# Performance work log

Hardware: AMD Instinct MI355X
Metric: run time of the kernel (lower is better)

The kernel has to match this reference:

```python
import jax, jax.numpy as jnp
import numpy as np

B, S, D = 2, 2048, 4096
H, HKV, HD = 32, 8, 128          # heads, kv heads, head_dim
G = H // HKV                      # query groups per kv head
THETA = 10000.0


def setup_inputs() -> dict:
    key = jax.random.key(0)
    ks = jax.random.split(key, 6)
    s = 0.02
    return {
        "hidden_states": jax.random.normal(ks[0], (B, S, D), jnp.float32),
        "position_ids": jnp.broadcast_to(jnp.arange(S, dtype=jnp.int32), (B, S)),
        "attention_mask": jnp.ones((B, S), jnp.int32),
        "Wq": jax.random.normal(ks[1], (D, H * HD), jnp.float32) * s,
        "Wk": jax.random.normal(ks[2], (D, HKV * HD), jnp.float32) * s,
        "Wv": jax.random.normal(ks[3], (D, HKV * HD), jnp.float32) * s,
        "Wo": jax.random.normal(ks[4], (H * HD, D), jnp.float32) * s,
    }


def _rope_neox(x, positions):
    # x: [B, S, h, HD]; neox style: rotate halves
    half = HD // 2
    inv_freq = 1.0 / (THETA ** (jnp.arange(0, half, dtype=jnp.float32) / half))
    freqs = positions.astype(jnp.float32)[..., None] * inv_freq  # [B,S,half]
    cos = jnp.cos(freqs)[:, :, None, :]
    sin = jnp.sin(freqs)[:, :, None, :]
    x1, x2 = x[..., :half], x[..., half:]
    return jnp.concatenate([x1 * cos - x2 * sin, x2 * cos + x1 * sin], axis=-1)


def reference(hidden_states, position_ids, attention_mask, Wq, Wk, Wv, Wo):
    q = (hidden_states @ Wq).reshape(B, S, H, HD)
    k = (hidden_states @ Wk).reshape(B, S, HKV, HD)
    v = (hidden_states @ Wv).reshape(B, S, HKV, HD)

    q = _rope_neox(q, position_ids)
    k = _rope_neox(k, position_ids)

    # GQA: group query heads onto kv heads
    qg = q.reshape(B, S, HKV, G, HD)
    scale = HD ** -0.5
    scores = jnp.einsum("bqhgd,bkhd->bhgqk", qg, k) * scale  # [B,HKV,G,S,S]

    causal = jnp.tril(jnp.ones((S, S), bool))
    mask = causal[None, None, None] & (attention_mask[:, None, None, None, :] > 0)
    scores = jnp.where(mask, scores, jnp.finfo(scores.dtype).min)
    probs = jax.nn.softmax(scores, axis=-1)

    ctx = jnp.einsum("bhgqk,bkhd->bqhgd", probs, v).reshape(B, S, H * HD)
    return ctx @ Wo
```

## Files before the change

### kernel.cpp

```cpp
#include <hip/hip_runtime.h>
#include <hip/hip_bf16.h>
#include <cstdint>
#include <cstddef>

#define BB 2
#define SS 2048
#define DD 4096
#define HH 32
#define HKV 8
#define HDIM 128
#define NQKV 6144

typedef __attribute__((ext_vector_type(8))) short bf16x8;
typedef __attribute__((ext_vector_type(4))) float f32x4;

#define GLOAD_LDS16(g, l) __builtin_amdgcn_global_load_lds( \
    (const __attribute__((address_space(1))) void*)(g), \
    (__attribute__((address_space(3))) void*)(l), 16, 0, 0)

__global__ void cast_bf16_kernel(const float* __restrict__ in,
                                 __hip_bfloat16* __restrict__ out, int n4) {
  int i = blockIdx.x * 256 + threadIdx.x;
  if (i >= n4) return;
  float4 v = ((const float4*)in)[i];
  union { __hip_bfloat16 h[4]; short4 s4; } u;
  u.h[0] = __float2bfloat16(v.x);
  u.h[1] = __float2bfloat16(v.y);
  u.h[2] = __float2bfloat16(v.z);
  u.h[3] = __float2bfloat16(v.w);
  ((short4*)out)[i] = u.s4;
}

__global__ void transpose_cast4_kernel(const float* __restrict__ Wq,
                                       const float* __restrict__ Wk,
                                       const float* __restrict__ Wv,
                                       const float* __restrict__ Wo,
                                       __hip_bfloat16* __restrict__ WqkvT,
                                       __hip_bfloat16* __restrict__ WoT) {
  __shared__ float tile[32][33];
  int id = blockIdx.x;
  const float* W; __hip_bfloat16* WT; int C, bx, by;
  if (id < 16384)      { W = Wq; WT = WqkvT;                         C = 4096; int l = id;         bx = l & 127; by = l >> 7; }
  else if (id < 20480) { W = Wk; WT = WqkvT + (size_t)4096 * 4096;   C = 1024; int l = id - 16384; bx = l & 31;  by = l >> 5; }
  else if (id < 24576) { W = Wv; WT = WqkvT + (size_t)5120 * 4096;   C = 1024; int l = id - 20480; bx = l & 31;  by = l >> 5; }
  else                 { W = Wo; WT = WoT;                           C = 4096; int l = id - 24576; bx = l & 127; by = l >> 7; }
  const int R = 4096;
  int c0 = bx * 32, r0 = by * 32;
  int tx = threadIdx.x, ty = threadIdx.y;
#pragma unroll
  for (int i = 0; i < 32; i += 8)
    tile[ty + i][tx] = W[(size_t)(r0 + ty + i) * C + c0 + tx];
  __syncthreads();
#pragma unroll
  for (int i = 0; i < 32; i += 8)
    WT[(size_t)(c0 + ty + i) * R + r0 + tx] = __float2bfloat16(tile[tx][ty + i]);
}

__global__ void vt_kernel(const __hip_bfloat16* __restrict__ QKV,
                          __hip_bfloat16* __restrict__ VT) {
  __shared__ __hip_bfloat16 tile[32][33];
  int c0 = blockIdx.x * 32;
  int r0 = blockIdx.y * 32;
  int tx = threadIdx.x, ty = threadIdx.y;
#pragma unroll
  for (int i = 0; i < 32; i += 8)
    tile[ty + i][tx] = QKV[(size_t)(r0 + ty + i) * NQKV + 5120 + c0 + tx];
  __syncthreads();
#pragma unroll
  for (int i = 0; i < 32; i += 8) {
    int r = r0 + tx;
    int c = c0 + ty + i;
    VT[((size_t)(r >> 11) * 1024 + c) * SS + (r & 2047)] = tile[tx][ty + i];
  }
}

__global__ void rope_kernel(__hip_bfloat16* __restrict__ QKV,
                            const int* __restrict__ pos_ids) {
  int r = blockIdx.x;
  float fpos = (float)pos_ids[r];
  __hip_bfloat16* row = QKV + (size_t)r * NQKV;
  for (int p = threadIdx.x; p < 2560; p += 256) {
    int base, i;
    if (p < 2048) { base = (p >> 6) * HDIM; i = p & 63; }
    else { int q = p - 2048; base = DD + (q >> 6) * HDIM; i = q & 63; }
    float inv = exp2f(-(float)i * 0.20762050593046015f);
    float f = fpos * inv;
    float c = cosf(f), s = sinf(f);
    float x1 = __bfloat162float(row[base + i]);
    float x2 = __bfloat162float(row[base + i + 64]);
    row[base + i]      = __float2bfloat16(x1 * c - x2 * s);
    row[base + i + 64] = __float2bfloat16(x2 * c + x1 * s);
  }
}

template <int OUTF32>
__global__ __launch_bounds__(256) void gemm_bt_kernel(const __hip_bfloat16* __restrict__ A,
                                                      const __hip_bfloat16* __restrict__ BT,
                                                      void* __restrict__ Cout,
                                                      int M, int N, int K) {
  __shared__ alignas(16) __hip_bfloat16 As[128 * 32];
  __shared__ alignas(16) __hip_bfloat16 Bs[128 * 32];
  int bn = blockIdx.x, bm = blockIdx.y;
  int tid = threadIdx.x, wave = tid >> 6, lane = tid & 63;
  int lr = lane & 15, lq = lane >> 4;
  int wm = (wave >> 1) * 64, wn = (wave & 1) * 64;
  int row0 = bm * 128, col0 = bn * 128;
  int swz = lq ^ ((lr >> 1) & 3);
  f32x4 acc[4][4] = {};
  for (int k0 = 0; k0 < K; k0 += 32) {
    __syncthreads();
#pragma unroll
    for (int i = 0; i < 2; ++i) {
      int c = tid + i * 256;
      int r = c >> 2, cl = c & 3;
      int cg = cl ^ ((r >> 1) & 3);
      GLOAD_LDS16(A + (size_t)(row0 + r) * K + k0 + cg * 8, As + (size_t)c * 8);
      GLOAD_LDS16(BT + (size_t)(col0 + r) * K + k0 + cg * 8, Bs + (size_t)c * 8);
    }
    __syncthreads();
    bf16x8 af[4], bfb[4];
#pragma unroll
    for (int mt = 0; mt < 4; ++mt)
      af[mt] = *(const bf16x8*)(As + ((wm + mt * 16 + lr) * 4 + swz) * 8);
#pragma unroll
    for (int nt = 0; nt < 4; ++nt)
      bfb[nt] = *(const bf16x8*)(Bs + ((wn + nt * 16 + lr) * 4 + swz) * 8);
#pragma unroll
    for (int mt = 0; mt < 4; ++mt)
#pragma unroll
      for (int nt = 0; nt < 4; ++nt)
        acc[mt][nt] = __builtin_amdgcn_mfma_f32_16x16x32_bf16(af[mt], bfb[nt], acc[mt][nt], 0, 0, 0);
  }
#pragma unroll
  for (int mt = 0; mt < 4; ++mt)
#pragma unroll
    for (int nt = 0; nt < 4; ++nt)
#pragma unroll
      for (int r = 0; r < 4; ++r) {
        int row = row0 + wm + mt * 16 + lq * 4 + r;
        int col = col0 + wn + nt * 16 + lr;
        if (OUTF32) ((float*)Cout)[(size_t)row * N + col] = acc[mt][nt][r];
        else ((__hip_bfloat16*)Cout)[(size_t)row * N + col] = __float2bfloat16(acc[mt][nt][r]);
      }
}

#define PSTRIDE 72
__global__ __launch_bounds__(256) void attn_kernel(const __hip_bfloat16* __restrict__ QKV,
                                                   const __hip_bfloat16* __restrict__ VT,
                                                   __hip_bfloat16* __restrict__ Ctx) {
  __shared__ alignas(16) __hip_bfloat16 Ks[64 * 128];
  __shared__ alignas(16) __hip_bfloat16 Vs[128 * 64];
  __shared__ alignas(16) __hip_bfloat16 Ps[4][32 * PSTRIDE];
  int h = blockIdx.y, b = blockIdx.z;
  int hkv = h >> 2;
  int tid = threadIdx.x, wave = tid >> 6, lane = tid & 63;
  int lr = lane & 15, lq = lane >> 4;
  const __hip_bfloat16* Kbase = QKV + (size_t)b * SS * NQKV + DD + hkv * HDIM;
  const __hip_bfloat16* Vbase = VT + (size_t)(b * HKV + hkv) * HDIM * SS;
  const float scale = 0.08838834764831845f;

  for (int half = 0; half < 2; ++half) {
    int qt = half ? (15 - blockIdx.x) : blockIdx.x;
    int q0 = qt * 128 + wave * 32;

    bf16x8 qfrag[2][4];
#pragma unroll
    for (int mt = 0; mt < 2; ++mt) {
      const __hip_bfloat16* qrow = QKV + (size_t)(b * SS + q0 + mt * 16 + lr) * NQKV + h * HDIM;
#pragma unroll
      for (int ks = 0; ks < 4; ++ks) qfrag[mt][ks] = *(const bf16x8*)(qrow + ks * 32 + lq * 8);
    }

    f32x4 accO[2][8] = {};
    float m_r[2][4], l_r[2][4];
#pragma unroll
    for (int mt = 0; mt < 2; ++mt)
#pragma unroll
      for (int r = 0; r < 4; ++r) { m_r[mt][r] = -1e30f; l_r[mt][r] = 0.f; }

    int kv_end = qt * 128 + 128;
    for (int kv0 = 0; kv0 < kv_end; kv0 += 64) {
      __syncthreads();
#pragma unroll
      for (int i = 0; i < 4; ++i) {
        int c = tid + i * 256;
        int r = c >> 4, cl = c & 15, cg = cl ^ (r & 15);
        GLOAD_LDS16(Kbase + (size_t)(kv0 + r) * NQKV + cg * 8, Ks + (size_t)c * 8);
      }
#pragma unroll
      for (int i = 0; i < 4; ++i) {
        int c = tid + i * 256;
        int r = c >> 3, cl = c & 7, cg = cl ^ (r & 7);
        GLOAD_LDS16(Vbase + (size_t)r * SS + kv0 + cg * 8, Vs + (size_t)c * 8);
      }
      __syncthreads();

      f32x4 sc[2][4] = {};
#pragma unroll
      for (int nt = 0; nt < 4; ++nt)
#pragma unroll
        for (int ks = 0; ks < 4; ++ks) {
          int cl = (ks * 4 + lq) ^ lr;
          bf16x8 kf = *(const bf16x8*)(Ks + ((nt * 16 + lr) * 16 + cl) * 8);
#pragma unroll
          for (int mt = 0; mt < 2; ++mt)
            sc[mt][nt] = __builtin_amdgcn_mfma_f32_16x16x32_bf16(qfrag[mt][ks], kf, sc[mt][nt], 0, 0, 0);
        }

      if (kv0 + 64 > qt * 128) {
#pragma unroll
        for (int mt = 0; mt < 2; ++mt)
#pragma unroll
          for (int nt = 0; nt < 4; ++nt)
#pragma unroll
            for (int r = 0; r < 4; ++r) {
              float v = sc[mt][nt][r] * scale;
              int qp = q0 + mt * 16 + lq * 4 + r;
              int kp = kv0 + nt * 16 + lr;
              sc[mt][nt][r] = (kp > qp) ? -1e30f : v;
            }
      } else {
#pragma unroll
        for (int mt = 0; mt < 2; ++mt)
#pragma unroll
          for (int nt = 0; nt < 4; ++nt)
#pragma unroll
            for (int r = 0; r < 4; ++r) sc[mt][nt][r] *= scale;
      }

      float alpha[2][4];
#pragma unroll
      for (int mt = 0; mt < 2; ++mt)
#pragma unroll
        for (int r = 0; r < 4; ++r) {
          float mx = fmaxf(fmaxf(sc[mt][0][r], sc[mt][1][r]), fmaxf(sc[mt][2][r], sc[mt][3][r]));
#pragma unroll
          for (int d = 1; d < 16; d <<= 1) mx = fmaxf(mx, __shfl_xor(mx, d));
          float mnew = fmaxf(m_r[mt][r], mx);
          alpha[mt][r] = __expf(m_r[mt][r] - mnew);
          m_r[mt][r] = mnew;
        }
#pragma unroll
      for (int mt = 0; mt < 2; ++mt)
#pragma unroll
        for (int nt = 0; nt < 4; ++nt)
#pragma unroll
          for (int r = 0; r < 4; ++r) sc[mt][nt][r] = __expf(sc[mt][nt][r] - m_r[mt][r]);
#pragma unroll
      for (int mt = 0; mt < 2; ++mt)
#pragma unroll
        for (int r = 0; r < 4; ++r) {
          float sm = (sc[mt][0][r] + sc[mt][1][r]) + (sc[mt][2][r] + sc[mt][3][r]);
#pragma unroll
          for (int d = 1; d < 16; d <<= 1) sm += __shfl_xor(sm, d);
          l_r[mt][r] = l_r[mt][r] * alpha[mt][r] + sm;
        }
#pragma unroll
      for (int mt = 0; mt < 2; ++mt)
#pragma unroll
        for (int t = 0; t < 8; ++t)
#pragma unroll
          for (int r = 0; r < 4; ++r) accO[mt][t][r] *= alpha[mt][r];

      __hip_bfloat16* P = Ps[wave];
#pragma unroll
      for (int mt = 0; mt < 2; ++mt)
#pragma unroll
        for (int nt = 0; nt < 4; ++nt)
#pragma unroll
          for (int r = 0; r < 4; ++r)
            P[(mt * 16 + lq * 4 + r) * PSTRIDE + nt * 16 + lr] = __float2bfloat16(sc[mt][nt][r]);

#pragma unroll
      for (int ks2 = 0; ks2 < 2; ++ks2) {
        bf16x8 pf[2];
#pragma unroll
        for (int mt = 0; mt < 2; ++mt)
          pf[mt] = *(const bf16x8*)(P + (mt * 16 + lr) * PSTRIDE + ks2 * 32 + lq * 8);
#pragma unroll
        for (int t = 0; t < 8; ++t) {
          int cl = (ks2 * 4 + lq) ^ (lr & 7);
          bf16x8 vf = *(const bf16x8*)(Vs + ((t * 16 + lr) * 8 + cl) * 8);
#pragma unroll
          for (int mt = 0; mt < 2; ++mt)
            accO[mt][t] = __builtin_amdgcn_mfma_f32_16x16x32_bf16(pf[mt], vf, accO[mt][t], 0, 0, 0);
        }
      }
    }

#pragma unroll
    for (int mt = 0; mt < 2; ++mt)
#pragma unroll
      for (int t = 0; t < 8; ++t)
#pragma unroll
        for (int r = 0; r < 4; ++r) {
          float o = accO[mt][t][r] / l_r[mt][r];
          int row = q0 + mt * 16 + lq * 4 + r;
          int col = h * HDIM + t * 16 + lr;
          Ctx[(size_t)(b * SS + row) * (HH * HDIM) + col] = __float2bfloat16(o);
        }
  }
}

extern "C" void kernel_launch(void* const* d_in, const int* in_sizes, int n_in,
                              void* d_out, int out_size, void* d_ws, size_t ws_size,
                              hipStream_t stream) {
  const float* X  = (const float*)d_in[0];
  const int* pos  = (const int*)d_in[1];
  const float* Wq = (const float*)d_in[3];
  const float* Wk = (const float*)d_in[4];
  const float* Wv = (const float*)d_in[5];
  const float* Wo = (const float*)d_in[6];
  float* out = (float*)d_out;

  char* ws = (char*)d_ws;
  __hip_bfloat16* Xb    = (__hip_bfloat16*)(ws);
  __hip_bfloat16* Ctx   = (__hip_bfloat16*)(ws);
  __hip_bfloat16* WqkvT = (__hip_bfloat16*)(ws + 33554432);
  __hip_bfloat16* WoT   = (__hip_bfloat16*)(ws + 83886080);
  __hip_bfloat16* QKV   = (__hip_bfloat16*)(ws + 117440512);
  __hip_bfloat16* VT    = (__hip_bfloat16*)(ws + 167772160);

  const int n4 = (BB * SS * DD) / 4;
  cast_bf16_kernel<<<dim3(n4 / 256), dim3(256), 0, stream>>>(X, Xb, n4);

  transpose_cast4_kernel<<<dim3(40960), dim3(32, 8), 0, stream>>>(Wq, Wk, Wv, Wo, WqkvT, WoT);

  gemm_bt_kernel<0><<<dim3(6144 / 128, 4096 / 128), dim3(256), 0, stream>>>(Xb, WqkvT, QKV, 4096, 6144, 4096);

  rope_kernel<<<dim3(BB * SS), dim3(256), 0, stream>>>(QKV, pos);
  vt_kernel<<<dim3(1024 / 32, 4096 / 32), dim3(32, 8), 0, stream>>>(QKV, VT);

  attn_kernel<<<dim3(SS / 256, HH, BB), dim3(256), 0, stream>>>(QKV, VT, Ctx);

  gemm_bt_kernel<1><<<dim3(4096 / 128, 4096 / 128), dim3(256), 0, stream>>>(Ctx, WoT, out, 4096, 4096, 4096);
}
```

Measured before the change: 947.8 us.

## Use 32x32x16 MFMA with BK=64 in GEMM and shrink attention query tiles

The GEMM moves from 16x16x32 MFMA tiles with a K-step of 32 to 32x32x16 MFMA tiles with a K-step of 64 and a matching XOR swizzle. This halves the barrier count per K and cuts LDS fragment reads per MFMA. The attention kernel drops from 128 to 64 query rows per block (16 per wave) and doubles the grid. It adds a swizzled P buffer and a launch bound of 4 blocks per CU, aiming for more parallelism and lower register pressure. The cost is that each K/V tile loaded into LDS is now reused by fewer query rows, so K/V traffic per query row rises.

```diff
diff --git a/kernel.cpp b/kernel.cpp
--- a/kernel.cpp
+++ b/kernel.cpp
@@ -13,6 +13,7 @@
 
 typedef __attribute__((ext_vector_type(8))) short bf16x8;
 typedef __attribute__((ext_vector_type(4))) float f32x4;
+typedef __attribute__((ext_vector_type(16))) float f32x16;
 
 #define GLOAD_LDS16(g, l) __builtin_amdgcn_global_load_lds( \
     (const __attribute__((address_space(1))) void*)(g), \
@@ -98,59 +99,64 @@
                                                       const __hip_bfloat16* __restrict__ BT,
                                                       void* __restrict__ Cout,
                                                       int M, int N, int K) {
-  __shared__ alignas(16) __hip_bfloat16 As[128 * 32];
-  __shared__ alignas(16) __hip_bfloat16 Bs[128 * 32];
+  __shared__ alignas(16) __hip_bfloat16 As[128 * 64];
+  __shared__ alignas(16) __hip_bfloat16 Bs[128 * 64];
   int bn = blockIdx.x, bm = blockIdx.y;
   int tid = threadIdx.x, wave = tid >> 6, lane = tid & 63;
-  int lr = lane & 15, lq = lane >> 4;
+  int lm = lane & 31, lh = lane >> 5;
   int wm = (wave >> 1) * 64, wn = (wave & 1) * 64;
   int row0 = bm * 128, col0 = bn * 128;
-  int swz = lq ^ ((lr >> 1) & 3);
-  f32x4 acc[4][4] = {};
-  for (int k0 = 0; k0 < K; k0 += 32) {
+  f32x16 acc[2][2] = {};
+  for (int k0 = 0; k0 < K; k0 += 64) {
     __syncthreads();
 #pragma unroll
-    for (int i = 0; i < 2; ++i) {
+    for (int i = 0; i < 4; ++i) {
       int c = tid + i * 256;
-      int r = c >> 2, cl = c & 3;
-      int cg = cl ^ ((r >> 1) & 3);
+      int r = c >> 3, cl = c & 7;
+      int cg = cl ^ (r & 7);
       GLOAD_LDS16(A + (size_t)(row0 + r) * K + k0 + cg * 8, As + (size_t)c * 8);
       GLOAD_LDS16(BT + (size_t)(col0 + r) * K + k0 + cg * 8, Bs + (size_t)c * 8);
     }
     __syncthreads();
-    bf16x8 af[4], bfb[4];
-#pragma unroll
-    for (int mt = 0; mt < 4; ++mt)
-      af[mt] = *(const bf16x8*)(As + ((wm + mt * 16 + lr) * 4 + swz) * 8);
-#pragma unroll
-    for (int nt = 0; nt < 4; ++nt)
-      bfb[nt] = *(const bf16x8*)(Bs + ((wn + nt * 16 + lr) * 4 + swz) * 8);
-#pragma unroll
-    for (int mt = 0; mt < 4; ++mt)
-#pragma unroll
-      for (int nt = 0; nt < 4; ++nt)
-        acc[mt][nt] = __builtin_amdgcn_mfma_f32_16x16x32_bf16(af[mt], bfb[nt], acc[mt][nt], 0, 0, 0);
+#pragma unroll
+    for (int ks = 0; ks < 4; ++ks) {
+      bf16x8 af[2], bfb[2];
+#pragma unroll
+      for (int mt = 0; mt < 2; ++mt) {
+        int cl = (ks * 2 + lh) ^ (lm & 7);
+        af[mt] = *(const bf16x8*)(As + (wm + mt * 32 + lm) * 64 + cl * 8);
+      }
+#pragma unroll
+      for (int nt = 0; nt < 2; ++nt) {
+        int cl = (ks * 2 + lh) ^ (lm & 7);
+        bfb[nt] = *(const bf16x8*)(Bs + (wn + nt * 32 + lm) * 64 + cl * 8);
+      }
+#pragma unroll
+      for (int mt = 0; mt < 2; ++mt)
+#pragma unroll
+        for (int nt = 0; nt < 2; ++nt)
+          acc[mt][nt] = __builtin_amdgcn_mfma_f32_32x32x16_bf16(af[mt], bfb[nt], acc[mt][nt], 0, 0, 0);
+    }
   }
 #pragma unroll
-  for (int mt = 0; mt < 4; ++mt)
-#pragma unroll
-    for (int nt = 0; nt < 4; ++nt)
-#pragma unroll
-      for (int r = 0; r < 4; ++r) {
-        int row = row0 + wm + mt * 16 + lq * 4 + r;
-        int col = col0 + wn + nt * 16 + lr;
+  for (int mt = 0; mt < 2; ++mt)
+#pragma unroll
+    for (int nt = 0; nt < 2; ++nt)
+#pragma unroll
+      for (int r = 0; r < 16; ++r) {
+        int row = row0 + wm + mt * 32 + (r & 3) + 8 * (r >> 2) + 4 * lh;
+        int col = col0 + wn + nt * 32 + lm;
         if (OUTF32) ((float*)Cout)[(size_t)row * N + col] = acc[mt][nt][r];
         else ((__hip_bfloat16*)Cout)[(size_t)row * N + col] = __float2bfloat16(acc[mt][nt][r]);
       }
 }
 
-#define PSTRIDE 72
-__global__ __launch_bounds__(256) void attn_kernel(const __hip_bfloat16* __restrict__ QKV,
-                                                   const __hip_bfloat16* __restrict__ VT,
-                                                   __hip_bfloat16* __restrict__ Ctx) {
+__global__ __launch_bounds__(256, 4) void attn_kernel(const __hip_bfloat16* __restrict__ QKV,
+                                                      const __hip_bfloat16* __restrict__ VT,
+                                                      __hip_bfloat16* __restrict__ Ctx) {
   __shared__ alignas(16) __hip_bfloat16 Ks[64 * 128];
   __shared__ alignas(16) __hip_bfloat16 Vs[128 * 64];
-  __shared__ alignas(16) __hip_bfloat16 Ps[4][32 * PSTRIDE];
+  __shared__ alignas(16) __hip_bfloat16 Ps[4][16 * 64];
   int h = blockIdx.y, b = blockIdx.z;
   int hkv = h >> 2;
   int tid = threadIdx.x, wave = tid >> 6, lane = tid & 63;
@@ -160,25 +166,19 @@
   const float scale = 0.08838834764831845f;
 
   for (int half = 0; half < 2; ++half) {
-    int qt = half ? (15 - blockIdx.x) : blockIdx.x;
-    int q0 = qt * 128 + wave * 32;
-
-    bf16x8 qfrag[2][4];
-#pragma unroll
-    for (int mt = 0; mt < 2; ++mt) {
-      const __hip_bfloat16* qrow = QKV + (size_t)(b * SS + q0 + mt * 16 + lr) * NQKV + h * HDIM;
-#pragma unroll
-      for (int ks = 0; ks < 4; ++ks) qfrag[mt][ks] = *(const bf16x8*)(qrow + ks * 32 + lq * 8);
-    }
-
-    f32x4 accO[2][8] = {};
-    float m_r[2][4], l_r[2][4];
-#pragma unroll
-    for (int mt = 0; mt < 2; ++mt)
-#pragma unroll
-      for (int r = 0; r < 4; ++r) { m_r[mt][r] = -1e30f; l_r[mt][r] = 0.f; }
-
-    int kv_end = qt * 128 + 128;
+    int qt = half ? (31 - blockIdx.x) : blockIdx.x;
+    int q0 = qt * 64 + wave * 16;
+
+    const __hip_bfloat16* qrow = QKV + (size_t)(b * SS + q0 + lr) * NQKV + h * HDIM;
+    bf16x8 qfrag[4];
+#pragma unroll
+    for (int ks = 0; ks < 4; ++ks) qfrag[ks] = *(const bf16x8*)(qrow + ks * 32 + lq * 8);
+
+    f32x4 accO[8] = {};
+    float m_r[4] = {-1e30f, -1e30f, -1e30f, -1e30f};
+    float l_r[4] = {0.f, 0.f, 0.f, 0.f};
+
+    int kv_end = qt * 64 + 64;
     for (int kv0 = 0; kv0 < kv_end; kv0 += 64) {
       __syncthreads();
 #pragma unroll
@@ -195,110 +195,90 @@
       }
       __syncthreads();
 
-      f32x4 sc[2][4] = {};
+      f32x4 sc[4] = {};
 #pragma unroll
       for (int nt = 0; nt < 4; ++nt)
 #pragma unroll
         for (int ks = 0; ks < 4; ++ks) {
           int cl = (ks * 4 + lq) ^ lr;
           bf16x8 kf = *(const bf16x8*)(Ks + ((nt * 16 + lr) * 16 + cl) * 8);
-#pragma unroll
-          for (int mt = 0; mt < 2; ++mt)
-            sc[mt][nt] = __builtin_amdgcn_mfma_f32_16x16x32_bf16(qfrag[mt][ks], kf, sc[mt][nt], 0, 0, 0);
+          sc[nt] = __builtin_amdgcn_mfma_f32_16x16x32_bf16(qfrag[ks], kf, sc[nt], 0, 0, 0);
         }
 
-      if (kv0 + 64 > qt * 128) {
-#pragma unroll
-        for (int mt = 0; mt < 2; ++mt)
-#pragma unroll
-          for (int nt = 0; nt < 4; ++nt)
-#pragma unroll
-            for (int r = 0; r < 4; ++r) {
-              float v = sc[mt][nt][r] * scale;
-              int qp = q0 + mt * 16 + lq * 4 + r;
-              int kp = kv0 + nt * 16 + lr;
-              sc[mt][nt][r] = (kp > qp) ? -1e30f : v;
-            }
+      if (kv0 + 64 > qt * 64) {
+#pragma unroll
+        for (int nt = 0; nt < 4; ++nt)
+#pragma unroll
+          for (int r = 0; r < 4; ++r) {
+            float v = sc[nt][r] * scale;
+            int qp = q0 + lq * 4 + r;
+            int kp = kv0 + nt * 16 + lr;
+            sc[nt][r] = (kp > qp) ? -1e30f : v;
+          }
       } else {
 #pragma unroll
-        for (int mt = 0; mt < 2; ++mt)
-#pragma unroll
-          for (int nt = 0; nt < 4; ++nt)
-#pragma unroll
-            for (int r = 0; r < 4; ++r) sc[mt][nt][r] *= scale;
-      }
-
-      float alpha[2][4];
-#pragma unroll
-      for (int mt = 0; mt < 2; ++mt)
+        for (int nt = 0; nt < 4; ++nt)
+#pragma unroll
+          for (int r = 0; r < 4; ++r) sc[nt][r] *= scale;
+      }
+
+      float alpha[4];
+#pragma unroll
+      for (int r = 0; r < 4; ++r) {
+        float mx = fmaxf(fmaxf(sc[0][r], sc[1][r]), fmaxf(sc[2][r], sc[3][r]));
+#pragma unroll
+        for (int d = 1; d < 16; d <<= 1) mx = fmaxf(mx, __shfl_xor(mx, d));
+        float mnew = fmaxf(m_r[r], mx);
+        alpha[r] = __expf(m_r[r] - mnew);
+        m_r[r] = mnew;
+      }
+#pragma unroll
+      for (int nt = 0; nt < 4; ++nt)
+#pragma unroll
+        for (int r = 0; r < 4; ++r) sc[nt][r] = __expf(sc[nt][r] - m_r[r]);
+#pragma unroll
+      for (int r = 0; r < 4; ++r) {
+        float sm = (sc[0][r] + sc[1][r]) + (sc[2][r] + sc[3][r]);
+#pragma unroll
+        for (int d = 1; d < 16; d <<= 1) sm += __shfl_xor(sm, d);
+        l_r[r] = l_r[r] * alpha[r] + sm;
+      }
+#pragma unroll
+      for (int t = 0; t < 8; ++t)
+#pragma unroll
+        for (int r = 0; r < 4; ++r) accO[t][r] *= alpha[r];
+
+      __hip_bfloat16* P = Ps[wave];
+#pragma unroll
+      for (int nt = 0; nt < 4; ++nt)
 #pragma unroll
         for (int r = 0; r < 4; ++r) {
-          float mx = fmaxf(fmaxf(sc[mt][0][r], sc[mt][1][r]), fmaxf(sc[mt][2][r], sc[mt][3][r]));
-#pragma unroll
-          for (int d = 1; d < 16; d <<= 1) mx = fmaxf(mx, __shfl_xor(mx, d));
-          float mnew = fmaxf(m_r[mt][r], mx);
-          alpha[mt][r] = __expf(m_r[mt][r] - mnew);
-          m_r[mt][r] = mnew;
+          int row = lq * 4 + r;
+          int cs = (nt * 2 + (lr >> 3)) ^ (row & 7);
+          P[row * 64 + cs * 8 + (lr & 7)] = __float2bfloat16(sc[nt][r]);
         }
-#pragma unroll
-      for (int mt = 0; mt < 2; ++mt)
-#pragma unroll
-        for (int nt = 0; nt < 4; ++nt)
-#pragma unroll
-          for (int r = 0; r < 4; ++r) sc[mt][nt][r] = __expf(sc[mt][nt][r] - m_r[mt][r]);
-#pragma unroll
-      for (int mt = 0; mt < 2; ++mt)
-#pragma unroll
-        for (int r = 0; r < 4; ++r) {
-          float sm = (sc[mt][0][r] + sc[mt][1][r]) + (sc[mt][2][r] + sc[mt][3][r]);
-#pragma unroll
-          for (int d = 1; d < 16; d <<= 1) sm += __shfl_xor(sm, d);
-          l_r[mt][r] = l_r[mt][r] * alpha[mt][r] + sm;
-        }
-#pragma unroll
-      for (int mt = 0; mt < 2; ++mt)
-#pragma unroll
-        for (int t = 0; t < 8; ++t)
-#pragma unroll
-          for (int r = 0; r < 4; ++r) accO[mt][t][r] *= alpha[mt][r];
-
-      __hip_bfloat16* P = Ps[wave];
-#pragma unroll
-      for (int mt = 0; mt < 2; ++mt)
-#pragma unroll
-        for (int nt = 0; nt < 4; ++nt)
-#pragma unroll
-          for (int r = 0; r < 4; ++r)
-            P[(mt * 16 + lq * 4 + r) * PSTRIDE + nt * 16 + lr] = __float2bfloat16(sc[mt][nt][r]);
 
 #pragma unroll
       for (int ks2 = 0; ks2 < 2; ++ks2) {
-        bf16x8 pf[2];
-#pragma unroll
-        for (int mt = 0; mt < 2; ++mt)
-          pf[mt] = *(const bf16x8*)(P + (mt * 16 + lr) * PSTRIDE + ks2 * 32 + lq * 8);
+        bf16x8 pf = *(const bf16x8*)(P + lr * 64 + ((ks2 * 4 + lq) ^ (lr & 7)) * 8);
 #pragma unroll
         for (int t = 0; t < 8; ++t) {
           int cl = (ks2 * 4 + lq) ^ (lr & 7);
           bf16x8 vf = *(const bf16x8*)(Vs + ((t * 16 + lr) * 8 + cl) * 8);
-#pragma unroll
-          for (int mt = 0; mt < 2; ++mt)
-            accO[mt][t] = __builtin_amdgcn_mfma_f32_16x16x32_bf16(pf[mt], vf, accO[mt][t], 0, 0, 0);
+          accO[t] = __builtin_amdgcn_mfma_f32_16x16x32_bf16(pf, vf, accO[t], 0, 0, 0);
         }
       }
     }
 
 #pragma unroll
-    for (int mt = 0; mt < 2; ++mt)
-#pragma unroll
-      for (int t = 0; t < 8; ++t)
-#pragma unroll
-        for (int r = 0; r < 4; ++r) {
-          float o = accO[mt][t][r] / l_r[mt][r];
-          int row = q0 + mt * 16 + lq * 4 + r;
-          int col = h * HDIM + t * 16 + lr;
-          Ctx[(size_t)(b * SS + row) * (HH * HDIM) + col] = __float2bfloat16(o);
-        }
+    for (int t = 0; t < 8; ++t)
+#pragma unroll
+      for (int r = 0; r < 4; ++r) {
+        float o = accO[t][r] / l_r[r];
+        int row = q0 + lq * 4 + r;
+        int col = h * HDIM + t * 16 + lr;
+        Ctx[(size_t)(b * SS + row) * (HH * HDIM) + col] = __float2bfloat16(o);
+      }
   }
 }
 
@@ -331,7 +311,7 @@
   rope_kernel<<<dim3(BB * SS), dim3(256), 0, stream>>>(QKV, pos);
   vt_kernel<<<dim3(1024 / 32, 4096 / 32), dim3(32, 8), 0, stream>>>(QKV, VT);
 
-  attn_kernel<<<dim3(SS / 256, HH, BB), dim3(256), 0, stream>>>(QKV, VT, Ctx);
+  attn_kernel<<<dim3(SS / 128, HH, BB), dim3(256), 0, stream>>>(QKV, VT, Ctx);
 
   gemm_bt_kernel<1><<<dim3(4096 / 128, 4096 / 128), dim3(256), 0, stream>>>(Ctx, WoT, out, 4096, 4096, 4096);
 }
```

Result: no change. 956.9 us (+1.0%).
